# Kernel optimization log

Measured on AMD Instinct MI355X. Metric: run time of the kernel, lower is better.

## Reference

```python
import jax, jax.numpy as jnp
import numpy as np

N = 64
DX = np.pi / N
# torch.fft.fftfreq(N+1, d) == np.fft.fftfreq(N+1) / d ; d varies per env so keep base freqs
BASE_FREQ = (2.0 * np.pi * np.fft.fftfreq(N + 1)).astype(np.float32)  # [65]
DOMAIN = np.array([0.75, 1.0, 0.75, 1.0, 0.75, 1.0, 0.75, 1.0], dtype=np.float32)


def _poisson_solve(w, dx_b):
    # w: [B,N,N] vorticity (already negated), dx_b: [B]
    w_pad = jnp.pad(w, ((0, 0), (0, 1), (0, 1)), mode='wrap')          # circular pad (0,1,0,1) -> [B,65,65]
    wf = jnp.fft.fft2(w_pad / (N ** 2))
    f = BASE_FREQ[None, :] / dx_b[:, None]                             # [B,65] per-env wavenumbers
    k2 = f[:, :, None] ** 2 + f[:, None, :] ** 2                       # [B,65,65] (meshgrid 'ij': kxx^2+kyy^2)
    uf = -wf / (1e-12 + k2)
    uf = uf.at[:, 0, 0].set(0.0)
    return jnp.fft.ifft2((N ** 2) * uf).real[:, :N, :N]                # [B,N,N]


def reference(t, y0, env, params):
    x = y0[:, 0]                                                       # [B,N,N]
    env = env.astype(jnp.int32)
    mu = params[env, 0][:, None, None]                                 # [B,1,1]
    fdx = (jnp.asarray(DOMAIN)[env] * DX)[:, None, None]               # [B,1,1]

    psi = _poisson_solve(-x, fdx[:, 0, 0])

    dxp = lambda a: jnp.roll(a, -1, axis=2) - jnp.roll(a, 1, axis=2)   # derive_x
    dyp = lambda a: jnp.roll(a, -1, axis=1) - jnp.roll(a, 1, axis=1)   # derive_y
    inv4 = 1.0 / (4.0 * fdx ** 2)

    J1 = (dyp(psi) * dxp(x) - dxp(psi) * dyp(x)) * inv4
    J2 = (jnp.roll(x, -1, axis=2) * dyp(jnp.roll(psi, -1, axis=2))
          - jnp.roll(x, 1, axis=2) * dyp(jnp.roll(psi, 1, axis=2))
          - jnp.roll(x, -1, axis=1) * dxp(jnp.roll(psi, -1, axis=1))
          + jnp.roll(x, 1, axis=1) * dxp(jnp.roll(psi, 1, axis=1))) * inv4
    J3 = (jnp.roll(x, (-1, -1), axis=(1, 2)) * (jnp.roll(psi, -1, axis=1) - jnp.roll(psi, -1, axis=2))
          - jnp.roll(x, (1, 1), axis=(1, 2)) * (jnp.roll(psi, 1, axis=2) - jnp.roll(psi, 1, axis=1))
          - jnp.roll(x, (-1, 1), axis=(1, 2)) * (jnp.roll(psi, -1, axis=1) - jnp.roll(psi, 1, axis=2))
          + jnp.roll(x, (1, -1), axis=(1, 2)) * (jnp.roll(psi, -1, axis=2) - jnp.roll(psi, 1, axis=1))) * inv4

    # circular-pad conv2d with kernel [[0,1,0],[1,-4,1],[1,1,0]] == cross-correlation stencil below
    lap = (jnp.roll(x, 1, axis=1) + jnp.roll(x, -1, axis=1)
           + jnp.roll(x, 1, axis=2) + jnp.roll(x, -1, axis=2)
           + jnp.roll(x, (-1, 1), axis=(1, 2)) - 4.0 * x) / (fdx ** 2)

    dudt = -(J1 + J2 + J3) / 3.0 + mu * lap
    return dudt[:, None]                                               # [B,1,N,N]


def setup_inputs() -> dict:
    key = jax.random.key(0)
    k1, k2 = jax.random.split(key)
    B, n_env = 2048, 8
    y0 = jax.random.normal(k1, (B, 1, N, N), dtype=jnp.float32)
    env = jax.random.randint(k2, (B,), 0, n_env, dtype=jnp.int64)
    params = jnp.concatenate([jnp.full((n_env, 1), 0.005, jnp.float32),
                              jnp.full((n_env, 1), 1.0, jnp.float32)], axis=1)
    t = jnp.zeros((1,), dtype=jnp.float32)
    return {"t": t, "y0": y0, "env": env, "params": params}
```

## Files before the change

### kernel.cpp

```cpp
#include <hip/hip_runtime.h>
#include <math.h>

#define P65 65
#define PLANE_U16 5248
#define SIDE_OFF  5120
#define PSI_U16   8320

__device__ __align__(16) ushort gAfrag[18*512];
__device__ float  g_MpN[65*65];
__device__ float  g64tab[64];

__device__ __constant__ float c_DOMAIN[8] = {0.75f,1.0f,0.75f,1.0f,0.75f,1.0f,0.75f,1.0f};

__device__ inline ushort f2bf(float f) {
  unsigned u = __float_as_uint(f);
  return (ushort)((u + 0x7FFFu + ((u >> 16) & 1u)) >> 16);
}
__device__ inline float bf2f(ushort h) { return __uint_as_float(((unsigned)h) << 16); }

__device__ inline void barrier_lds() {
  asm volatile("s_waitcnt lgkmcnt(0)" ::: "memory");
  __builtin_amdgcn_sched_barrier(0);
  __builtin_amdgcn_s_barrier();
  __builtin_amdgcn_sched_barrier(0);
}

__device__ inline float Gvalf(int r, int i) {
  int m = (r <= 32) ? r : (r - 32);
  int prod = (m * (i % 65)) % 65;
  float ang = 6.2831853071795864769f * (float)prod / 65.0f;
  return (r <= 32) ? cosf(ang) : sinf(ang);
}
__device__ inline float Gfoldf(int r, int i) {
  float v = Gvalf(r, i);
  if (i == 0) v += Gvalf(r, 64);
  return v;
}

__global__ void init_tables() {
  int tid = blockIdx.x*blockDim.x + threadIdx.x;
  int nth = gridDim.x*blockDim.x;
  for (int idx = tid; idx < 18*512; idx += nth) {
    int blk = idx >> 9, rem = idx & 511;
    int lane = rem >> 3, e = rem & 7;
    int i16 = lane & 15, kg = lane >> 4;
    float v = 0.f;
    if (blk < 10) {
      int mt = blk >> 1, kt = blk & 1;
      int r = 16*mt + i16;
      int i = 32*kt + 8*kg + e;
      if (r < 65 && i < 64) v = Gfoldf(r, i);
    } else {
      int b2 = blk - 10;
      int mt = b2 >> 1, kt = b2 & 1;
      int j  = 16*mt + i16;
      int k1 = 32*kt + 8*kg + e;
      if (j < 64 && k1 < 64) v = Gvalf(k1, j);
    }
    gAfrag[idx] = f2bf(v);
  }
  for (int idx = tid; idx < 65*65; idx += nth) {
    int k1 = idx/65, k2 = idx%65;
    float v = 0.f;
    if (k1 | k2) {
      float n1 = (k1==0)?(1.0f/65.0f):(2.0f/65.0f);
      float n2 = (k2==0)?(1.0f/65.0f):(2.0f/65.0f);
      int m1 = (k1<=32)?k1:(k1-32), m2 = (k2<=32)?k2:(k2-32);
      float b1 = 6.2831853071795864769f*(float)m1/65.0f;
      float b2 = 6.2831853071795864769f*(float)m2/65.0f;
      v = (n1*n2)/(b1*b1 + b2*b2);
    }
    g_MpN[idx] = v;
  }
  for (int idx = tid; idx < 64; idx += nth)
    g64tab[idx] = Gvalf(64, idx);
}

typedef __attribute__((ext_vector_type(8))) short bf16x8;
typedef __attribute__((ext_vector_type(4))) float f32x4;

template<int MT, int NT, bool SCALE, bool RK>
struct Pre {
  bf16x8 af[2][2];
  float  mp[2][4];
  float  gv[2][4];
};

template<int MT, int NT, int TBLOFF, bool SCALE, bool RK>
__device__ inline void prefetch(Pre<MT,NT,SCALE,RK>& P, int wvu, int lane) {
  const int lg = lane >> 4, li = lane & 15;
  constexpr int NTL = MT*NT;
  #pragma unroll
  for (int tb = 0; tb < 2; ++tb) {
    int tile = wvu + 8*tb;
    int tl = (tile < NTL) ? tile : 0;
    int mt = tl / NT, nt = tl - mt*NT;
    #pragma unroll
    for (int kt = 0; kt < 2; ++kt)
      P.af[tb][kt] = *(const bf16x8*)(gAfrag + (TBLOFF + mt*2 + kt)*512 + lane*8);
    if (SCALE || RK) {
      int n = 16*nt + li;  int nc = (n <= 64) ? n : 64;
      int mb = 16*mt + 4*lg;
      #pragma unroll
      for (int r = 0; r < 4; ++r) {
        int m = mb + r;
        if (SCALE) P.mp[tb][r] = g_MpN[((m <= 64) ? m : 64)*65 + nc];
        if (RK)    P.gv[tb][r] = g64tab[(m <= 63) ? m : 63];
      }
    }
  }
}

template<int MT, int NT, int MR, int NR, int TBLOFF, bool SCALE, bool RK, bool PSI>
__device__ inline void stage(const Pre<MT,NT,SCALE,RK>& P,
                             const ushort* __restrict__ Lin,
                             ushort* __restrict__ Lout,
                             float* __restrict__ psiout,
                             int wvu, int lane)
{
  const int lg = lane >> 4, li = lane & 15;
  constexpr int NTL = MT*NT;
  constexpr int TPW = (NTL + 7) >> 3;
  #pragma unroll
  for (int tb = 0; tb < TPW; ++tb) {
    int tile = wvu + 8*tb;
    bool act = (tile < NTL);
    int tl = act ? tile : 0;
    int mt = tl / NT, nt = tl - mt*NT;
    int n = 16*nt + li;
    f32x4 acc = {0.f, 0.f, 0.f, 0.f};
    #pragma unroll
    for (int kt = 0; kt < 2; ++kt) {
      bf16x8 af = (tb < 2) ? P.af[tb][kt]
                           : *(const bf16x8*)(gAfrag + (TBLOFF + mt*2 + kt)*512 + lane*8);
      bf16x8 bfr = *(const bf16x8*)(Lin + (nt*2 + kt)*512 + lane*8);
      acc = __builtin_amdgcn_mfma_f32_16x16x32_bf16(af, bfr, acc, 0, 0, 0);
    }
    float rkB = 0.f;
    if (RK) rkB = bf2f(Lin[SIDE_OFF + n]);
    int mbase = 16*mt + 4*lg;
    int wbase = (mt*2 + (nt>>1))*512 + ((2*nt + (li>>3))&3)*128 + (li&7);
    #pragma unroll
    for (int r = 0; r < 4; ++r) {
      int m = mbase + r;
      if (act && m < MR && n < NR) {
        float v = acc[r];
        if (SCALE) v *= (tb < 2) ? P.mp[tb][r] : g_MpN[m*65 + n];
        if (RK)    v = fmaf((tb < 2) ? P.gv[tb][r] : g64tab[m], rkB, v);
        if (PSI) {
          psiout[n*P65 + m] = v;
        } else if (NT == 5 && nt == 4) {
          Lout[SIDE_OFF + m] = f2bf(v);
        } else {
          Lout[wbase + (4*lg + r)*8] = f2bf(v);
        }
      }
    }
  }
}

__device__ inline float shflx(float v, int srclane) { return __shfl(v, srclane, 64); }

__global__ void __launch_bounds__(512) pde_main(const float* __restrict__ y0,
                                                const int*   __restrict__ env,
                                                const float* __restrict__ params,
                                                float*       __restrict__ out)
{
  __shared__ __align__(16) ushort Lsh[PLANE_U16 + PSI_U16];
  ushort* PB   = Lsh;
  ushort* PA   = Lsh + PLANE_U16;
  float*  Ppsi = (float*)(Lsh + PLANE_U16);

  const int b    = blockIdx.x;
  const int t    = threadIdx.x;
  const int lane = t & 63;
  const int wvu  = __builtin_amdgcn_readfirstlane(t >> 6);

  const int   e       = env[b];
  const float mu      = params[2*e];
  const float fdx     = c_DOMAIN[e] * (float)(3.14159265358979323846/64.0);
  const float inv_dx2 = 1.0f/(fdx*fdx);

  const float* xb = y0 + (size_t)b*4096;

  const int j0 = wvu*8, jm0 = (j0+63)&63, jp8 = (j0+8)&63;
  float xbm = xb[jm0*64 + lane];
  float xbp = xb[jp8*64 + lane];

  float xr[8];
  bf16x8 hv;
  #pragma unroll
  for (int k=0;k<8;++k) {
    float v = xb[(8*wvu + k)*64 + lane];
    xr[k] = v;
    hv[k] = (short)f2bf(v);
  }
  {
    int wb = ((lane>>4)*2 + (wvu>>2))*512 + ((wvu&3)*16 + (lane&15))*8;
    *(bf16x8*)(PA + wb) = hv;
  }
  Pre<5,4,false,false> p1;  prefetch<5,4,0,false,false>(p1, wvu, lane);
  barrier_lds();

  stage<5,4,65,64, 0,false,false,false>(p1, PA, PB, nullptr, wvu, lane);
  Pre<5,5,true,false> p2;  prefetch<5,5,0,true,false>(p2, wvu, lane);
  barrier_lds();

  stage<5,5,65,65, 0,true ,false,false>(p2, PB, PA, nullptr, wvu, lane);
  Pre<4,5,false,true> p3;  prefetch<4,5,10,false,true>(p3, wvu, lane);
  barrier_lds();

  stage<4,5,64,65,10,false,true ,false>(p3, PA, PB, nullptr, wvu, lane);
  Pre<4,4,false,true> p4;  prefetch<4,4,10,false,true>(p4, wvu, lane);
  barrier_lds();

  stage<4,4,64,64,10,false,true ,true >(p4, PB, nullptr, Ppsi, wvu, lane);
  barrier_lds();

  {
    const int c = lane, cm = (c+63)&63, cp = (c+1)&63;
    float* op = out + (size_t)b*4096;

    float xm_c = xbm,   xm_m = shflx(xm_c, cm), xm_p = shflx(xm_c, cp);
    float xc_c = xr[0], xc_m = shflx(xc_c, cm), xc_p = shflx(xc_c, cp);
    float pm_m = Ppsi[jm0*P65+cm], pm_c = Ppsi[jm0*P65+c], pm_p = Ppsi[jm0*P65+cp];
    float pc_m = Ppsi[j0 *P65+cm], pc_c = Ppsi[j0 *P65+c], pc_p = Ppsi[j0 *P65+cp];

    #pragma unroll
    for (int m=0;m<8;++m) {
      int j = j0 + m, jp = (j+1)&63;
      float xn_c = (m < 7) ? xr[m+1] : xbp;
      float xn_m = shflx(xn_c, cm), xn_p = shflx(xn_c, cp);
      float pn_m = Ppsi[jp*P65+cm], pn_c = Ppsi[jp*P65+c], pn_p = Ppsi[jp*P65+cp];

      float J1 = (pn_c - pm_c)*(xc_p - xc_m) - (pc_p - pc_m)*(xn_c - xm_c);
      float J2 = xc_p*(pn_p - pm_p) - xc_m*(pn_m - pm_m)
               - xn_c*(pn_p - pn_m) + xm_c*(pm_p - pm_m);
      float J3 = xn_p*(pn_c - pc_p) - xm_m*(pc_m - pm_c)
               - xn_m*(pn_c - pc_m) + xm_p*(pc_p - pm_c);
      float lap = (xm_c + xn_c + xc_m + xc_p + xn_m - 4.0f*xc_c) * inv_dx2;

      op[j*64 + c] = -(J1 + J2 + J3)*(0.25f/3.0f) + mu*lap;

      xm_m=xc_m; xm_c=xc_c; xm_p=xc_p;  pm_m=pc_m; pm_c=pc_c; pm_p=pc_p;
      xc_m=xn_m; xc_c=xn_c; xc_p=xn_p;  pc_m=pn_m; pc_c=pn_c; pc_p=pn_p;
    }
  }
}

extern "C" void kernel_launch(void* const* d_in, const int* in_sizes, int n_in,
                              void* d_out, int out_size, void* d_ws, size_t ws_size,
                              hipStream_t stream) {
  const float* y0     = (const float*)d_in[1];
  const int*   env    = (const int*)  d_in[2];
  const float* params = (const float*)d_in[3];
  float*       out    = (float*)d_out;
  int B = in_sizes[1] / 4096;

  init_tables<<<64, 256, 0, stream>>>();
  pde_main<<<B, 512, 0, stream>>>(y0, env, params, out);
}
```

Measured before the change: 40.92 us.

## Transpose MFMA operand roles so epilogue stores and scale loads are vectorized

Swaps the A/B operands of every DFT MFMA stage so the accumulator rows run along the data dimension. The per-lane epilogue can then load four scale factors with one f32x4 read from a padded transposed table, read the side-column values as one uint2, and write four packed bf16 outputs with one 8-byte LDS store instead of four scalar stores. Inactive tiles are skipped with an early continue, and the final stencil indexes psi in the transposed layout. This cuts scalar LDS and global traffic in the epilogues, but changes the layout of every intermediate, so any indexing mistake would give wrong results.

Result: faster. 34.97 us (-14.5%).

```diff
diff --git a/kernel.cpp b/kernel.cpp
--- a/kernel.cpp
+++ b/kernel.cpp
@@ -7,8 +7,8 @@
 #define PSI_U16   8320
 
 __device__ __align__(16) ushort gAfrag[18*512];
-__device__ float  g_MpN[65*65];
-__device__ float  g64tab[64];
+__device__ float  g_MpPad[65*68];
+__device__ float  g64tab[65];
 
 __device__ __constant__ float c_DOMAIN[8] = {0.75f,1.0f,0.75f,1.0f,0.75f,1.0f,0.75f,1.0f};
 
@@ -59,10 +59,10 @@
     }
     gAfrag[idx] = f2bf(v);
   }
-  for (int idx = tid; idx < 65*65; idx += nth) {
-    int k1 = idx/65, k2 = idx%65;
+  for (int idx = tid; idx < 65*68; idx += nth) {
+    int k2 = idx/68, k1 = idx%68;
     float v = 0.f;
-    if (k1 | k2) {
+    if (k1 <= 64 && (k1 | k2)) {
       float n1 = (k1==0)?(1.0f/65.0f):(2.0f/65.0f);
       float n2 = (k2==0)?(1.0f/65.0f):(2.0f/65.0f);
       int m1 = (k1<=32)?k1:(k1-32), m2 = (k2<=32)?k2:(k2-32);
@@ -70,90 +70,91 @@
       float b2 = 6.2831853071795864769f*(float)m2/65.0f;
       v = (n1*n2)/(b1*b1 + b2*b2);
     }
-    g_MpN[idx] = v;
-  }
-  for (int idx = tid; idx < 64; idx += nth)
-    g64tab[idx] = Gvalf(64, idx);
+    g_MpPad[idx] = v;
+  }
+  for (int idx = tid; idx < 65; idx += nth)
+    g64tab[idx] = (idx < 64) ? Gvalf(64, idx) : 0.f;
 }
 
 typedef __attribute__((ext_vector_type(8))) short bf16x8;
 typedef __attribute__((ext_vector_type(4))) float f32x4;
 
-template<int MT, int NT, bool SCALE, bool RK>
-struct Pre {
-  bf16x8 af[2][2];
-  float  mp[2][4];
-  float  gv[2][4];
-};
-
-template<int MT, int NT, int TBLOFF, bool SCALE, bool RK>
-__device__ inline void prefetch(Pre<MT,NT,SCALE,RK>& P, int wvu, int lane) {
-  const int lg = lane >> 4, li = lane & 15;
-  constexpr int NTL = MT*NT;
+template<int JT, int TBLOFF>
+__device__ inline void prefetchA(bf16x8 (&pre)[2][2], int wvu, int lane, int NTL) {
   #pragma unroll
   for (int tb = 0; tb < 2; ++tb) {
     int tile = wvu + 8*tb;
     int tl = (tile < NTL) ? tile : 0;
-    int mt = tl / NT, nt = tl - mt*NT;
+    int jt = tl % JT;
     #pragma unroll
     for (int kt = 0; kt < 2; ++kt)
-      P.af[tb][kt] = *(const bf16x8*)(gAfrag + (TBLOFF + mt*2 + kt)*512 + lane*8);
-    if (SCALE || RK) {
-      int n = 16*nt + li;  int nc = (n <= 64) ? n : 64;
-      int mb = 16*mt + 4*lg;
-      #pragma unroll
-      for (int r = 0; r < 4; ++r) {
-        int m = mb + r;
-        if (SCALE) P.mp[tb][r] = g_MpN[((m <= 64) ? m : 64)*65 + nc];
-        if (RK)    P.gv[tb][r] = g64tab[(m <= 63) ? m : 63];
-      }
-    }
-  }
-}
-
-template<int MT, int NT, int MR, int NR, int TBLOFF, bool SCALE, bool RK, bool PSI>
-__device__ inline void stage(const Pre<MT,NT,SCALE,RK>& P,
+      pre[tb][kt] = *(const bf16x8*)(gAfrag + (TBLOFF + jt*2 + kt)*512 + lane*8);
+  }
+}
+
+template<int IT, int JT, int TBLOFF, bool SCALE, bool RK, bool PSI>
+__device__ inline void stage(const bf16x8 (&pre)[2][2],
                              const ushort* __restrict__ Lin,
                              ushort* __restrict__ Lout,
                              float* __restrict__ psiout,
                              int wvu, int lane)
 {
   const int lg = lane >> 4, li = lane & 15;
-  constexpr int NTL = MT*NT;
+  constexpr int NTL = IT*JT;
   constexpr int TPW = (NTL + 7) >> 3;
   #pragma unroll
   for (int tb = 0; tb < TPW; ++tb) {
-    int tile = wvu + 8*tb;
-    bool act = (tile < NTL);
-    int tl = act ? tile : 0;
-    int mt = tl / NT, nt = tl - mt*NT;
-    int n = 16*nt + li;
+    const int tile = wvu + 8*tb;
+    if (tile >= NTL) continue;
+    const int it = tile / JT, jt = tile - it*JT;
     f32x4 acc = {0.f, 0.f, 0.f, 0.f};
     #pragma unroll
     for (int kt = 0; kt < 2; ++kt) {
-      bf16x8 af = (tb < 2) ? P.af[tb][kt]
-                           : *(const bf16x8*)(gAfrag + (TBLOFF + mt*2 + kt)*512 + lane*8);
-      bf16x8 bfr = *(const bf16x8*)(Lin + (nt*2 + kt)*512 + lane*8);
-      acc = __builtin_amdgcn_mfma_f32_16x16x32_bf16(af, bfr, acc, 0, 0, 0);
-    }
-    float rkB = 0.f;
-    if (RK) rkB = bf2f(Lin[SIDE_OFF + n]);
-    int mbase = 16*mt + 4*lg;
-    int wbase = (mt*2 + (nt>>1))*512 + ((2*nt + (li>>3))&3)*128 + (li&7);
-    #pragma unroll
-    for (int r = 0; r < 4; ++r) {
-      int m = mbase + r;
-      if (act && m < MR && n < NR) {
-        float v = acc[r];
-        if (SCALE) v *= (tb < 2) ? P.mp[tb][r] : g_MpN[m*65 + n];
-        if (RK)    v = fmaf((tb < 2) ? P.gv[tb][r] : g64tab[m], rkB, v);
-        if (PSI) {
-          psiout[n*P65 + m] = v;
-        } else if (NT == 5 && nt == 4) {
-          Lout[SIDE_OFF + m] = f2bf(v);
-        } else {
-          Lout[wbase + (4*lg + r)*8] = f2bf(v);
-        }
+      bf16x8 af = (tb < 2) ? pre[tb][kt]
+                           : *(const bf16x8*)(gAfrag + (TBLOFF + jt*2 + kt)*512 + lane*8);
+      bf16x8 df = *(const bf16x8*)(Lin + (it*2 + kt)*512 + lane*8);
+      acc = __builtin_amdgcn_mfma_f32_16x16x32_bf16(df, af, acc, 0, 0, 0);
+    }
+    const int f     = 16*jt + li;
+    const int dbase = 16*it + 4*lg;
+    const bool dEdge = (IT == 5) && (it == IT-1);
+    const bool fEdge = (JT == 5) && (jt == JT-1);
+
+    float v[4];
+    #pragma unroll
+    for (int r = 0; r < 4; ++r) v[r] = acc[r];
+
+    if (SCALE) {
+      const float* mp = g_MpPad + (fEdge ? 64 : f)*68 + (dEdge ? 64 : dbase);
+      if (dEdge) v[0] *= mp[0];
+      else {
+        f32x4 m4 = *(const f32x4*)mp;
+        #pragma unroll
+        for (int r = 0; r < 4; ++r) v[r] *= m4[r];
+      }
+    }
+    if (RK) {
+      float gv = g64tab[f];
+      uint2 sc = *(const uint2*)(Lin + SIDE_OFF + dbase);
+      v[0] = fmaf(bf2f((ushort)(sc.x      )), gv, v[0]);
+      v[1] = fmaf(bf2f((ushort)(sc.x >> 16)), gv, v[1]);
+      v[2] = fmaf(bf2f((ushort)(sc.y      )), gv, v[2]);
+      v[3] = fmaf(bf2f((ushort)(sc.y >> 16)), gv, v[3]);
+    }
+
+    if (PSI) {
+      #pragma unroll
+      for (int r = 0; r < 4; ++r) psiout[f*65 + dbase + r] = v[r];
+    } else if (dEdge) {
+      if (lg == 0 && (!fEdge || li == 0))
+        Lout[SIDE_OFF + f] = f2bf(v[0]);
+    } else {
+      if (!fEdge || li == 0) {
+        int wb = (2*jt + (it>>1))*512 + ((2*it + (lg>>1))&3)*128 + li*8 + 4*(lg&1);
+        uint2 pk;
+        pk.x = ((unsigned)f2bf(v[1]) << 16) | (unsigned)f2bf(v[0]);
+        pk.y = ((unsigned)f2bf(v[3]) << 16) | (unsigned)f2bf(v[2]);
+        *(uint2*)(Lout + wb) = pk;
       }
     }
   }
@@ -199,39 +200,40 @@
     int wb = ((lane>>4)*2 + (wvu>>2))*512 + ((wvu&3)*16 + (lane&15))*8;
     *(bf16x8*)(PA + wb) = hv;
   }
-  Pre<5,4,false,false> p1;  prefetch<5,4,0,false,false>(p1, wvu, lane);
-  barrier_lds();
-
-  stage<5,4,65,64, 0,false,false,false>(p1, PA, PB, nullptr, wvu, lane);
-  Pre<5,5,true,false> p2;  prefetch<5,5,0,true,false>(p2, wvu, lane);
-  barrier_lds();
-
-  stage<5,5,65,65, 0,true ,false,false>(p2, PB, PA, nullptr, wvu, lane);
-  Pre<4,5,false,true> p3;  prefetch<4,5,10,false,true>(p3, wvu, lane);
-  barrier_lds();
-
-  stage<4,5,64,65,10,false,true ,false>(p3, PA, PB, nullptr, wvu, lane);
-  Pre<4,4,false,true> p4;  prefetch<4,4,10,false,true>(p4, wvu, lane);
-  barrier_lds();
-
-  stage<4,4,64,64,10,false,true ,true >(p4, PB, nullptr, Ppsi, wvu, lane);
+  bf16x8 p1[2][2];  prefetchA<5,0>(p1, wvu, lane, 20);
+  barrier_lds();
+
+  stage<4,5, 0,false,false,false>(p1, PA, PB, nullptr, wvu, lane);
+  bf16x8 p2[2][2];  prefetchA<5,0>(p2, wvu, lane, 25);
+  barrier_lds();
+
+  stage<5,5, 0,true ,false,false>(p2, PB, PA, nullptr, wvu, lane);
+  bf16x8 p3[2][2];  prefetchA<4,10>(p3, wvu, lane, 20);
+  barrier_lds();
+
+  stage<5,4,10,false,true ,false>(p3, PA, PB, nullptr, wvu, lane);
+  bf16x8 p4[2][2];  prefetchA<4,10>(p4, wvu, lane, 16);
+  barrier_lds();
+
+  stage<4,4,10,false,true ,true >(p4, PB, nullptr, Ppsi, wvu, lane);
   barrier_lds();
 
   {
     const int c = lane, cm = (c+63)&63, cp = (c+1)&63;
+    const int cB = c*65, cmB = cm*65, cpB = cp*65;
     float* op = out + (size_t)b*4096;
 
     float xm_c = xbm,   xm_m = shflx(xm_c, cm), xm_p = shflx(xm_c, cp);
     float xc_c = xr[0], xc_m = shflx(xc_c, cm), xc_p = shflx(xc_c, cp);
-    float pm_m = Ppsi[jm0*P65+cm], pm_c = Ppsi[jm0*P65+c], pm_p = Ppsi[jm0*P65+cp];
-    float pc_m = Ppsi[j0 *P65+cm], pc_c = Ppsi[j0 *P65+c], pc_p = Ppsi[j0 *P65+cp];
+    float pm_m = Ppsi[cmB+jm0], pm_c = Ppsi[cB+jm0], pm_p = Ppsi[cpB+jm0];
+    float pc_m = Ppsi[cmB+j0 ], pc_c = Ppsi[cB+j0 ], pc_p = Ppsi[cpB+j0 ];
 
     #pragma unroll
     for (int m=0;m<8;++m) {
       int j = j0 + m, jp = (j+1)&63;
       float xn_c = (m < 7) ? xr[m+1] : xbp;
       float xn_m = shflx(xn_c, cm), xn_p = shflx(xn_c, cp);
-      float pn_m = Ppsi[jp*P65+cm], pn_c = Ppsi[jp*P65+c], pn_p = Ppsi[jp*P65+cp];
+      float pn_m = Ppsi[cmB+jp], pn_c = Ppsi[cB+jp], pn_p = Ppsi[cpB+jp];
 
       float J1 = (pn_c - pm_c)*(xc_p - xc_m) - (pc_p - pc_m)*(xn_c - xm_c);
       float J2 = xc_p*(pn_p - pm_p) - xc_m*(pn_m - pm_m)
```
